# Kernel optimization log

Measured on AMD Instinct MI355X. Metric: run time of the kernel, lower is better.

## Reference

```python
import jax, jax.numpy as jnp
import numpy as np

NUM_EMBEDDINGS = 1024
EMBEDDING_DIM = 256
COMMITMENT_COST = 0.25


def setup_inputs() -> dict:
    key = jax.random.key(0)
    k1, k2 = jax.random.split(key)
    z_e = jax.random.normal(k1, (32, 256, 32, 32), dtype=jnp.float32)
    # nn.init.uniform_(weight, -1/K, 1/K)
    bound = 1.0 / NUM_EMBEDDINGS
    weight = jax.random.uniform(k2, (NUM_EMBEDDINGS, EMBEDDING_DIM), dtype=jnp.float32,
                                minval=-bound, maxval=bound)
    return {"z_e": z_e, "weight": weight}


def reference(z_e, weight):
    B, C, H, W = z_e.shape
    sg = jax.lax.stop_gradient
    # (B, H, W, C) -> (N, C)
    flat = jnp.transpose(z_e, (0, 2, 3, 1)).reshape(-1, C)
    # squared L2 distances to each codebook vector: (N, K)
    dist = (jnp.sum(flat * flat, axis=1, keepdims=True)
            - 2.0 * flat @ weight.T
            + jnp.sum(weight * weight, axis=1))
    indices = jnp.argmin(dist, axis=1)  # (N,)
    # codebook lookup (equivalent to one-hot @ weight)
    quantized = weight[indices].reshape(B, H, W, C)
    quantized = jnp.transpose(quantized, (0, 3, 1, 2))  # (B, C, H, W)
    e_latent = jnp.mean((sg(quantized) - z_e) ** 2)
    q_latent = jnp.mean((quantized - sg(z_e)) ** 2)
    loss = q_latent + COMMITMENT_COST * e_latent
    # straight-through estimator
    quantized_st = z_e + sg(quantized - z_e)
    # codebook usage perplexity: avg_probs = mean of one-hot encodings
    n = flat.shape[0]
    counts = jax.ops.segment_sum(jnp.ones((n,), dtype=z_e.dtype), indices,
                                 num_segments=NUM_EMBEDDINGS)
    avg_probs = counts / n
    perplexity = jnp.exp(-jnp.sum(avg_probs * jnp.log(avg_probs + 1e-10)))
    return (quantized_st, loss, perplexity)
```

## Files before the change

kernel.cpp:

```cpp
#include <hip/hip_runtime.h>
#include <float.h>
#include <math.h>
#include <stdint.h>


#define NB   32
#define NC   256
#define NHW  1024
#define NK   1024
#define NELEM (NB*NC*NHW)

typedef __attribute__((ext_vector_type(8))) short bf16x8;
typedef __attribute__((ext_vector_type(4))) float f32x4;

__device__ __forceinline__ unsigned short f2bf(float f) {
    unsigned u = __float_as_uint(f);
    u += 0x7FFFu + ((u >> 16) & 1u);
    return (unsigned short)(u >> 16);
}

__global__ __launch_bounds__(256) void vq_wsq(const float* __restrict__ w,
                                              float* __restrict__ wsq) {
    const int lane = threadIdx.x & 63;
    const int wave = threadIdx.x >> 6;
    const int k = blockIdx.x * 4 + wave;
    const float* row = w + k * NC;
    float s = 0.f;
#pragma unroll
    for (int p = 0; p < 4; ++p) {
        float v = row[lane + p * 64];
        s = fmaf(v, v, s);
    }
#pragma unroll
    for (int off = 32; off; off >>= 1) s += __shfl_down(s, off, 64);
    if (lane == 0) wsq[k] = s;
}

__global__ __launch_bounds__(256) void vq_pack(const float* __restrict__ w,
                                               unsigned short* __restrict__ cb) {
    const int t = blockIdx.x;
#pragma unroll
    for (int rep = 0; rep < 2; ++rep) {
        const int p = threadIdx.x + rep * 256;
        const int cc = p >> 6, l = p & 63;
        const int n = l & 15, quad = l >> 4;
        const float* src = w + (t * 16 + n) * NC + cc * 32 + quad * 8;
        const float4 f0 = *(const float4*)src;
        const float4 f1 = *(const float4*)(src + 4);
        union { unsigned short u[8]; uint4 v; } pk;
        pk.u[0] = f2bf(-2.f * f0.x); pk.u[1] = f2bf(-2.f * f0.y);
        pk.u[2] = f2bf(-2.f * f0.z); pk.u[3] = f2bf(-2.f * f0.w);
        pk.u[4] = f2bf(-2.f * f1.x); pk.u[5] = f2bf(-2.f * f1.y);
        pk.u[6] = f2bf(-2.f * f1.z); pk.u[7] = f2bf(-2.f * f1.w);
        *(uint4*)(cb + (size_t)t * 4096 + cc * 512 + l * 8) = pk.v;
    }
}

__global__ __launch_bounds__(512) void vq_main2(const float* __restrict__ z,
                                                const float* __restrict__ w,
                                                const float* __restrict__ wsq,
                                                const unsigned short* __restrict__ cb,
                                                unsigned int* __restrict__ counts,
                                                float* __restrict__ loss_sum,
                                                float* __restrict__ out) {
    __shared__ __align__(16) char cbuf[2][32768];
    int*   fidx = (int*)cbuf[0];
    float* lred = (float*)(cbuf[0] + 1024);

    const int tid  = threadIdx.x;
    const int wv   = tid >> 6;
    const int lane = tid & 63;
    const int n    = lane & 15;
    const int quad = lane >> 4;
    const int bid  = blockIdx.x;
    const int b    = bid >> 3;
    const int hw0  = (bid & 7) << 7;
    const int hwb  = hw0 + wv * 16;

    const float* zb = z + (size_t)b * (NC * NHW);

    bf16x8 bfr[8];
#pragma unroll
    for (int cc = 0; cc < 8; ++cc) {
        const float* zp = zb + (size_t)(cc * 32 + quad * 8) * NHW + hwb + n;
        union { unsigned short u[8]; bf16x8 v; } pk;
#pragma unroll
        for (int j = 0; j < 8; ++j) pk.u[j] = f2bf(zp[(size_t)j * NHW]);
        bfr[cc] = pk.v;
    }

    const char* cbb = (const char*)cb;
#define STAGE(ch)                                                              \
    {                                                                          \
        const char* gsrc = cbb + (size_t)(ch) * 32768 + wv * 4096 + lane * 16; \
        char* ldst = cbuf[(ch) & 1] + wv * 4096;                               \
        _Pragma("unroll")                                                      \
        for (int i = 0; i < 4; ++i) {                                          \
            __builtin_amdgcn_global_load_lds(                                  \
                (const __attribute__((address_space(1))) unsigned int*)        \
                    (uintptr_t)(gsrc + i * 1024),                              \
                (__attribute__((address_space(3))) unsigned int*)              \
                    (uint32_t)(uintptr_t)(ldst + i * 1024),                    \
                16, 0, 0);                                                     \
        }                                                                      \
    }

    float bestv = FLT_MAX;
    int   besti = 0;

    STAGE(0);
    for (int ch = 0; ch < 16; ++ch) {
        __syncthreads();
        if (ch + 1 < 16) STAGE(ch + 1);
        const char* bufc = cbuf[ch & 1];
#pragma unroll
        for (int tp = 0; tp < 2; ++tp) {
            const int tt0 = tp * 2, tt1 = tp * 2 + 1;
            const int kt0 = (ch * 4 + tt0) * 16;
            const int kt1 = kt0 + 16;
            f32x4 acc0 = *(const f32x4*)(wsq + kt0 + quad * 4);
            f32x4 acc1 = *(const f32x4*)(wsq + kt1 + quad * 4);
#pragma unroll
            for (int cc = 0; cc < 8; ++cc) {
                bf16x8 a0 = *(const bf16x8*)(bufc + (tt0 * 8 + cc) * 1024 + lane * 16);
                bf16x8 a1 = *(const bf16x8*)(bufc + (tt1 * 8 + cc) * 1024 + lane * 16);
                acc0 = __builtin_amdgcn_mfma_f32_16x16x32_bf16(a0, bfr[cc], acc0, 0, 0, 0);
                acc1 = __builtin_amdgcn_mfma_f32_16x16x32_bf16(a1, bfr[cc], acc1, 0, 0, 0);
            }
#pragma unroll
            for (int r = 0; r < 4; ++r) {
                const float v0 = acc0[r];
                if (v0 < bestv) { bestv = v0; besti = kt0 + quad * 4 + r; }
                const float v1 = acc1[r];
                if (v1 < bestv) { bestv = v1; besti = kt1 + quad * 4 + r; }
            }
        }
    }

#pragma unroll
    for (int off = 16; off <= 32; off <<= 1) {
        const float ov = __shfl_xor(bestv, off, 64);
        const int   ok = __shfl_xor(besti, off, 64);
        if (ov < bestv || (ov == bestv && ok < besti)) { bestv = ov; besti = ok; }
    }
    __syncthreads();
    if (lane < 16) fidx[wv * 16 + lane] = besti;
    __syncthreads();
    if (tid < 128) atomicAdd(&counts[fidx[tid]], 1u);

    float lsum = 0.f;
    const int hwl = tid & 127;
    const int cg  = tid >> 7;
    const int myk = fidx[hwl];
    const float* wr  = w + myk * NC;
    const float* zp2 = zb + hw0 + hwl;
    float*       op  = out + (size_t)b * (NC * NHW) + hw0 + hwl;
#pragma unroll 4
    for (int p = 0; p < 16; ++p) {
        const int c0 = cg * 64 + p * 4;
        const float4 q4 = *(const float4*)(wr + c0);
        const float qa[4] = {q4.x, q4.y, q4.z, q4.w};
#pragma unroll
        for (int u = 0; u < 4; ++u) {
            const int c = c0 + u;
            const float zv = zp2[(size_t)c * NHW];
            const float d = qa[u] - zv;
            lsum = fmaf(d, d, lsum);
            op[(size_t)c * NHW] = qa[u];
        }
    }
#pragma unroll
    for (int off = 32; off; off >>= 1) lsum += __shfl_down(lsum, off, 64);
    if (lane == 0) lred[wv] = lsum;
    __syncthreads();
    if (tid == 0) {
        float t = 0.f;
#pragma unroll
        for (int i = 0; i < 8; ++i) t += lred[i];
        atomicAdd(loss_sum, t);
    }
}

__global__ __launch_bounds__(256) void vq_final(const unsigned int* __restrict__ counts,
                                                const float* __restrict__ loss_sum,
                                                float* __restrict__ out) {
    __shared__ float red[4];
    const int tid = threadIdx.x;
    float s = 0.f;
#pragma unroll
    for (int p = 0; p < 4; ++p) {
        const float pr = (float)counts[tid + p * 256] * (1.f / 32768.f);
        s = fmaf(pr, logf(pr + 1e-10f), s);
    }
#pragma unroll
    for (int off = 32; off; off >>= 1) s += __shfl_down(s, off, 64);
    if ((tid & 63) == 0) red[tid >> 6] = s;
    __syncthreads();
    if (tid == 0) {
        const float tot = red[0] + red[1] + red[2] + red[3];
        out[NELEM]     = loss_sum[0] * (1.25f / (float)NELEM);
        out[NELEM + 1] = expf(-tot);
    }
}

extern "C" void kernel_launch(void* const* d_in, const int* in_sizes, int n_in,
                              void* d_out, int out_size, void* d_ws, size_t ws_size,
                              hipStream_t stream) {
    const float* z = (const float*)d_in[0];
    const float* w = (const float*)d_in[1];
    float* out = (float*)d_out;

    float*          wsq      = (float*)d_ws;
    unsigned int*   counts   = (unsigned int*)((char*)d_ws + 4096);
    float*          loss_sum = (float*)((char*)d_ws + 8192);
    unsigned short* cbfrag   = (unsigned short*)((char*)d_ws + 16384);

    hipMemsetAsync((char*)d_ws + 4096, 0, 4100, stream);

    vq_wsq  <<<256, 256, 0, stream>>>(w, wsq);
    vq_pack <<<64,  256, 0, stream>>>(w, cbfrag);
    vq_main2<<<256, 512, 0, stream>>>(z, w, wsq, cbfrag, counts, loss_sum, out);
    vq_final<<<1,   256, 0, stream>>>(counts, loss_sum, out);
}
```

Before: 130.7 us.

## Split codebook across waves, drop LDS staging, fuse prep kernels

The main kernel is restructured so each block handles 64 spatial positions with 4 waves. Each wave holds all 64 positions' z fragments in registers and scans its own quarter of the codebook, reading fragments straight from global memory instead of double-buffering them through LDS. The per-wave argmin results are merged in shared memory. The weight-norm and pack kernels are merged into one prep kernel that also zeroes counts and the loss, which removes the memset and one launch. Register pressure rises from holding 32 bf16x8 fragments per lane, and every wave now does its own global codebook reads.

```diff
diff --git a/kernel.cpp b/kernel.cpp
--- a/kernel.cpp
+++ b/kernel.cpp
@@ -19,29 +19,18 @@
     return (unsigned short)(u >> 16);
 }
 
-__global__ __launch_bounds__(256) void vq_wsq(const float* __restrict__ w,
-                                              float* __restrict__ wsq) {
-    const int lane = threadIdx.x & 63;
-    const int wave = threadIdx.x >> 6;
-    const int k = blockIdx.x * 4 + wave;
-    const float* row = w + k * NC;
-    float s = 0.f;
-#pragma unroll
-    for (int p = 0; p < 4; ++p) {
-        float v = row[lane + p * 64];
-        s = fmaf(v, v, s);
-    }
-#pragma unroll
-    for (int off = 32; off; off >>= 1) s += __shfl_down(s, off, 64);
-    if (lane == 0) wsq[k] = s;
-}
-
-__global__ __launch_bounds__(256) void vq_pack(const float* __restrict__ w,
-                                               unsigned short* __restrict__ cb) {
-    const int t = blockIdx.x;
+__global__ __launch_bounds__(256) void vq_prep(const float* __restrict__ w,
+                                               unsigned short* __restrict__ cb,
+                                               float* __restrict__ wsq,
+                                               unsigned int* __restrict__ counts,
+                                               float* __restrict__ loss_sum) {
+    __shared__ float swsq[4][16];
+    const int t   = blockIdx.x;
+    const int tid = threadIdx.x;
+    float sq = 0.f;
 #pragma unroll
     for (int rep = 0; rep < 2; ++rep) {
-        const int p = threadIdx.x + rep * 256;
+        const int p = tid + rep * 256;
         const int cc = p >> 6, l = p & 63;
         const int n = l & 15, quad = l >> 4;
         const float* src = w + (t * 16 + n) * NC + cc * 32 + quad * 8;
@@ -53,19 +42,35 @@
         pk.u[4] = f2bf(-2.f * f1.x); pk.u[5] = f2bf(-2.f * f1.y);
         pk.u[6] = f2bf(-2.f * f1.z); pk.u[7] = f2bf(-2.f * f1.w);
         *(uint4*)(cb + (size_t)t * 4096 + cc * 512 + l * 8) = pk.v;
-    }
-}
-
-__global__ __launch_bounds__(512) void vq_main2(const float* __restrict__ z,
-                                                const float* __restrict__ w,
-                                                const float* __restrict__ wsq,
-                                                const unsigned short* __restrict__ cb,
-                                                unsigned int* __restrict__ counts,
-                                                float* __restrict__ loss_sum,
-                                                float* __restrict__ out) {
-    __shared__ __align__(16) char cbuf[2][32768];
-    int*   fidx = (int*)cbuf[0];
-    float* lred = (float*)(cbuf[0] + 1024);
+        sq = fmaf(f0.x, f0.x, sq); sq = fmaf(f0.y, f0.y, sq);
+        sq = fmaf(f0.z, f0.z, sq); sq = fmaf(f0.w, f0.w, sq);
+        sq = fmaf(f1.x, f1.x, sq); sq = fmaf(f1.y, f1.y, sq);
+        sq = fmaf(f1.z, f1.z, sq); sq = fmaf(f1.w, f1.w, sq);
+    }
+    sq += __shfl_xor(sq, 16, 64);
+    sq += __shfl_xor(sq, 32, 64);
+    const int wv = tid >> 6, lane = tid & 63;
+    if (lane < 16) swsq[wv][lane] = sq;
+    __syncthreads();
+    if (tid < 16)
+        wsq[t * 16 + tid] = swsq[0][tid] + swsq[1][tid] + swsq[2][tid] + swsq[3][tid];
+    if (t == 0) {
+        for (int i = tid; i < NK; i += 256) counts[i] = 0u;
+        if (tid == 0) loss_sum[0] = 0.f;
+    }
+}
+
+__global__ __launch_bounds__(256, 2) void vq_main3(const float* __restrict__ z,
+                                                   const float* __restrict__ w,
+                                                   const float* __restrict__ wsq,
+                                                   const unsigned short* __restrict__ cb,
+                                                   unsigned int* __restrict__ counts,
+                                                   float* __restrict__ loss_sum,
+                                                   float* __restrict__ out) {
+    __shared__ float sval[4][64];
+    __shared__ int   sidx[4][64];
+    __shared__ int   fidx[64];
+    __shared__ float lred[4];
 
     const int tid  = threadIdx.x;
     const int wv   = tid >> 6;
@@ -73,84 +78,88 @@
     const int n    = lane & 15;
     const int quad = lane >> 4;
     const int bid  = blockIdx.x;
-    const int b    = bid >> 3;
-    const int hw0  = (bid & 7) << 7;
-    const int hwb  = hw0 + wv * 16;
+    const int b    = bid >> 4;
+    const int hw0  = (bid & 15) << 6;
 
     const float* zb = z + (size_t)b * (NC * NHW);
 
-    bf16x8 bfr[8];
-#pragma unroll
-    for (int cc = 0; cc < 8; ++cc) {
-        const float* zp = zb + (size_t)(cc * 32 + quad * 8) * NHW + hwb + n;
-        union { unsigned short u[8]; bf16x8 v; } pk;
-#pragma unroll
-        for (int j = 0; j < 8; ++j) pk.u[j] = f2bf(zp[(size_t)j * NHW]);
-        bfr[cc] = pk.v;
-    }
-
-    const char* cbb = (const char*)cb;
-#define STAGE(ch)                                                              \
-    {                                                                          \
-        const char* gsrc = cbb + (size_t)(ch) * 32768 + wv * 4096 + lane * 16; \
-        char* ldst = cbuf[(ch) & 1] + wv * 4096;                               \
-        _Pragma("unroll")                                                      \
-        for (int i = 0; i < 4; ++i) {                                          \
-            __builtin_amdgcn_global_load_lds(                                  \
-                (const __attribute__((address_space(1))) unsigned int*)        \
-                    (uintptr_t)(gsrc + i * 1024),                              \
-                (__attribute__((address_space(3))) unsigned int*)              \
-                    (uint32_t)(uintptr_t)(ldst + i * 1024),                    \
-                16, 0, 0);                                                     \
-        }                                                                      \
-    }
-
-    float bestv = FLT_MAX;
-    int   besti = 0;
-
-    STAGE(0);
-    for (int ch = 0; ch < 16; ++ch) {
-        __syncthreads();
-        if (ch + 1 < 16) STAGE(ch + 1);
-        const char* bufc = cbuf[ch & 1];
-#pragma unroll
-        for (int tp = 0; tp < 2; ++tp) {
-            const int tt0 = tp * 2, tt1 = tp * 2 + 1;
-            const int kt0 = (ch * 4 + tt0) * 16;
-            const int kt1 = kt0 + 16;
-            f32x4 acc0 = *(const f32x4*)(wsq + kt0 + quad * 4);
-            f32x4 acc1 = *(const f32x4*)(wsq + kt1 + quad * 4);
-#pragma unroll
-            for (int cc = 0; cc < 8; ++cc) {
-                bf16x8 a0 = *(const bf16x8*)(bufc + (tt0 * 8 + cc) * 1024 + lane * 16);
-                bf16x8 a1 = *(const bf16x8*)(bufc + (tt1 * 8 + cc) * 1024 + lane * 16);
-                acc0 = __builtin_amdgcn_mfma_f32_16x16x32_bf16(a0, bfr[cc], acc0, 0, 0, 0);
-                acc1 = __builtin_amdgcn_mfma_f32_16x16x32_bf16(a1, bfr[cc], acc1, 0, 0, 0);
+    bf16x8 bfr[4][8];
+#pragma unroll
+    for (int nt = 0; nt < 4; ++nt) {
+#pragma unroll
+        for (int cc = 0; cc < 8; ++cc) {
+            const float* zp = zb + (size_t)(cc * 32 + quad * 8) * NHW + hw0 + nt * 16 + n;
+            union { unsigned short u[8]; bf16x8 v; } pk;
+#pragma unroll
+            for (int j = 0; j < 8; ++j) pk.u[j] = f2bf(zp[(size_t)j * NHW]);
+            bfr[nt][cc] = pk.v;
+        }
+    }
+
+    float bv[4] = {FLT_MAX, FLT_MAX, FLT_MAX, FLT_MAX};
+    int   bi[4] = {0, 0, 0, 0};
+    const unsigned short* ap0 = cb + (size_t)(wv * 16) * 4096 + lane * 8;
+
+    for (int mt = 0; mt < 16; ++mt) {
+        const int kt = wv * 256 + mt * 16;
+        const unsigned short* ap = ap0 + (size_t)mt * 4096;
+        const f32x4 w4 = *(const f32x4*)(wsq + kt + quad * 4);
+        f32x4 acc[4];
+#pragma unroll
+        for (int nt = 0; nt < 4; ++nt) acc[nt] = w4;
+#pragma unroll
+        for (int cc = 0; cc < 8; ++cc) {
+            const bf16x8 af = *(const bf16x8*)(ap + cc * 512);
+            acc[0] = __builtin_amdgcn_mfma_f32_16x16x32_bf16(af, bfr[0][cc], acc[0], 0, 0, 0);
+            acc[1] = __builtin_amdgcn_mfma_f32_16x16x32_bf16(af, bfr[1][cc], acc[1], 0, 0, 0);
+            acc[2] = __builtin_amdgcn_mfma_f32_16x16x32_bf16(af, bfr[2][cc], acc[2], 0, 0, 0);
+            acc[3] = __builtin_amdgcn_mfma_f32_16x16x32_bf16(af, bfr[3][cc], acc[3], 0, 0, 0);
+        }
+#pragma unroll
+        for (int nt = 0; nt < 4; ++nt) {
+#pragma unroll
+            for (int r = 0; r < 4; ++r) {
+                const float v = acc[nt][r];
+                if (v < bv[nt]) { bv[nt] = v; bi[nt] = kt + quad * 4 + r; }
             }
-#pragma unroll
-            for (int r = 0; r < 4; ++r) {
-                const float v0 = acc0[r];
-                if (v0 < bestv) { bestv = v0; besti = kt0 + quad * 4 + r; }
-                const float v1 = acc1[r];
-                if (v1 < bestv) { bestv = v1; besti = kt1 + quad * 4 + r; }
-            }
-        }
-    }
-
-#pragma unroll
-    for (int off = 16; off <= 32; off <<= 1) {
-        const float ov = __shfl_xor(bestv, off, 64);
-        const int   ok = __shfl_xor(besti, off, 64);
-        if (ov < bestv || (ov == bestv && ok < besti)) { bestv = ov; besti = ok; }
-    }
-    __syncthreads();
-    if (lane < 16) fidx[wv * 16 + lane] = besti;
-    __syncthreads();
-    if (tid < 128) atomicAdd(&counts[fidx[tid]], 1u);
+        }
+    }
+
+#pragma unroll
+    for (int nt = 0; nt < 4; ++nt) {
+#pragma unroll
+        for (int off = 16; off <= 32; off <<= 1) {
+            const float ov = __shfl_xor(bv[nt], off, 64);
+            const int   ok = __shfl_xor(bi[nt], off, 64);
+            if (ov < bv[nt] || (ov == bv[nt] && ok < bi[nt])) { bv[nt] = ov; bi[nt] = ok; }
+        }
+    }
+    if (lane < 16) {
+#pragma unroll
+        for (int nt = 0; nt < 4; ++nt) {
+            sval[wv][nt * 16 + lane] = bv[nt];
+            sidx[wv][nt * 16 + lane] = bi[nt];
+        }
+    }
+    __syncthreads();
+
+    if (tid < 64) {
+        float bestv = sval[0][tid];
+        int   besti = sidx[0][tid];
+#pragma unroll
+        for (int q = 1; q < 4; ++q) {
+            const float v = sval[q][tid];
+            const int   k = sidx[q][tid];
+            if (v < bestv || (v == bestv && k < besti)) { bestv = v; besti = k; }
+        }
+        fidx[tid] = besti;
+        atomicAdd(&counts[besti], 1u);
+    }
+    __syncthreads();
 
     float lsum = 0.f;
-    const int hwl = tid & 127;
-    const int cg  = tid >> 7;
+    const int hwl = tid & 63;
+    const int cg  = tid >> 6;
     const int myk = fidx[hwl];
     const float* wr  = w + myk * NC;
     const float* zp2 = zb + hw0 + hwl;
@@ -173,12 +182,8 @@
     for (int off = 32; off; off >>= 1) lsum += __shfl_down(lsum, off, 64);
     if (lane == 0) lred[wv] = lsum;
     __syncthreads();
-    if (tid == 0) {
-        float t = 0.f;
-#pragma unroll
-        for (int i = 0; i < 8; ++i) t += lred[i];
-        atomicAdd(loss_sum, t);
-    }
+    if (tid == 0)
+        atomicAdd(loss_sum, lred[0] + lred[1] + lred[2] + lred[3]);
 }
 
 __global__ __launch_bounds__(256) void vq_final(const unsigned int* __restrict__ counts,
@@ -215,10 +220,7 @@
     float*          loss_sum = (float*)((char*)d_ws + 8192);
     unsigned short* cbfrag   = (unsigned short*)((char*)d_ws + 16384);
 
-    hipMemsetAsync((char*)d_ws + 4096, 0, 4100, stream);
-
-    vq_wsq  <<<256, 256, 0, stream>>>(w, wsq);
-    vq_pack <<<64,  256, 0, stream>>>(w, cbfrag);
-    vq_main2<<<256, 512, 0, stream>>>(z, w, wsq, cbfrag, counts, loss_sum, out);
+    vq_prep <<<64,  256, 0, stream>>>(w, cbfrag, wsq, counts, loss_sum);
+    vq_main3<<<512, 256, 0, stream>>>(z, w, wsq, cbfrag, counts, loss_sum, out);
     vq_final<<<1,   256, 0, stream>>>(counts, loss_sum, out);
 }
```

Result: faster. 123.2 us (-5.7%).
